# Performance work log

Hardware: AMD Instinct MI355X
Metric: run time of the kernel (lower is better)

## Reference

```python
import jax, jax.numpy as jnp
import numpy as np

B, T, K = 512, 512, 64  # batch, seq_len, num_tags


def setup_inputs() -> dict:
    key = jax.random.key(0)
    k1, k2 = jax.random.split(key)
    inputs = jax.random.normal(k1, (B, T, K), dtype=jnp.float32)
    # learned CRF transition matrix (GlorotUniform-ish scale)
    transitions = jax.random.normal(k2, (K, K), dtype=jnp.float32) * 0.1
    return {"inputs": inputs, "transitions": transitions}


def _viterbi_decode(potentials, transitions, seq_lens):
    """Faithful jax version of tfa/tf crf_decode (max-plus Viterbi DP + backtrace).

    potentials: [B, T, K] unary scores
    transitions: [K, K] pairwise scores (from_tag, to_tag)
    seq_lens: [B] int valid lengths
    Returns (decode_tags [B, T] int32, best_score [B] float).
    """
    b, t, k = potentials.shape
    pots_t = jnp.transpose(potentials, (1, 0, 2))  # [T, B, K]
    # mask[t-1, b] = step t (1..T-1) is within sequence b
    mask = jnp.arange(1, t)[:, None] < seq_lens[None, :]  # [T-1, B]
    ident = jnp.arange(k, dtype=jnp.int32)

    def fwd_step(alpha, xs):
        pot_t, m = xs  # pot_t: [B, K], m: [B]
        scores = alpha[:, :, None] + transitions[None, :, :]  # [B, K_from, K_to]
        new_alpha = pot_t + jnp.max(scores, axis=1)           # [B, K]
        bp = jnp.argmax(scores, axis=1).astype(jnp.int32)     # [B, K]
        alpha = jnp.where(m[:, None], new_alpha, alpha)       # freeze past seq end
        bp = jnp.where(m[:, None], bp, ident[None, :])        # identity backptr
        return alpha, bp

    alpha0 = pots_t[0]
    alpha_final, bps = jax.lax.scan(fwd_step, alpha0, (pots_t[1:], mask))  # bps: [T-1, B, K]
    best_score = jnp.max(alpha_final, axis=1)                  # [B]
    last_tag = jnp.argmax(alpha_final, axis=1).astype(jnp.int32)  # [B]

    def back_step(tag, bp_t):
        prev = jnp.take_along_axis(bp_t, tag[:, None], axis=1)[:, 0]
        return prev, prev

    # reverse scan: ys[t] = best tag at time t, for t = 0..T-2
    _, prev_tags = jax.lax.scan(back_step, last_tag, bps, reverse=True)
    tags = jnp.concatenate([prev_tags, last_tag[None]], axis=0)  # [T, B]
    return jnp.transpose(tags), best_score


def reference(inputs, transitions):
    # sequence lengths derived exactly as in the original call()
    used = jnp.sign(jnp.abs(inputs))                       # [B, T, K]
    seq_lens = jnp.mean(jnp.sum(used, axis=1), axis=1)     # [B]
    seq_lens = seq_lens.astype(jnp.int32)
    decode_tags, _best_score = _viterbi_decode(inputs, transitions, seq_lens)
    return decode_tags
```

## Files before the change

### kernel.cpp

```cpp
#include <hip/hip_runtime.h>

#define BB 512
#define TT 512
#define KK 64

typedef float v2f __attribute__((ext_vector_type(2)));

__device__ __forceinline__ float frl(float v, int lane) {
    return __int_as_float(__builtin_amdgcn_readlane(__float_as_int(v), lane));
}
__device__ __forceinline__ float fmax3(float a, float b, float c) {
    float d;
    asm("v_max3_f32 %0, %1, %2, %3" : "=v"(d) : "v"(a), "v"(b), "v"(c));
    return d;
}

#define FSTEP(PT) do {                                                          \
    la[lane] = alpha;                                                           \
    asm volatile("" ::: "memory");                                              \
    float acc0, acc1, acc2, acc3;                                               \
    {                                                                           \
        float4 a4 = ((float4*)la)[0];                                           \
        v2f lo; lo.x = a4.x; lo.y = a4.y; v2f cl = lo + tcl[0];                 \
        v2f hi; hi.x = a4.z; hi.y = a4.w; v2f ch = hi + tch[0];                 \
        acc0 = fmaxf(cl.x, cl.y); acc1 = fmaxf(ch.x, ch.y);                     \
        a4 = ((float4*)la)[1];                                                  \
        lo.x = a4.x; lo.y = a4.y; cl = lo + tcl[1];                             \
        hi.x = a4.z; hi.y = a4.w; ch = hi + tch[1];                             \
        acc2 = fmaxf(cl.x, cl.y); acc3 = fmaxf(ch.x, ch.y);                     \
    }                                                                           \
    _Pragma("unroll")                                                           \
    for (int c = 2; c < 16; c += 2) {                                           \
        float4 a4 = ((float4*)la)[c];                                           \
        v2f lo; lo.x = a4.x; lo.y = a4.y; v2f cl = lo + tcl[c];                 \
        v2f hi; hi.x = a4.z; hi.y = a4.w; v2f ch = hi + tch[c];                 \
        acc0 = fmax3(acc0, cl.x, cl.y); acc1 = fmax3(acc1, ch.x, ch.y);         \
        a4 = ((float4*)la)[c + 1];                                              \
        lo.x = a4.x; lo.y = a4.y; cl = lo + tcl[c + 1];                         \
        hi.x = a4.z; hi.y = a4.w; ch = hi + tch[c + 1];                         \
        acc2 = fmax3(acc2, cl.x, cl.y); acc3 = fmax3(acc3, ch.x, ch.y);         \
    }                                                                           \
    float M = fmaxf(fmax3(acc0, acc1, acc2), acc3);                             \
    *hp = M; hp += KK;                                                          \
    alpha = (PT) + M;                                                           \
} while (0)

__global__ __launch_bounds__(64, 1) void crf_fused(const float* __restrict__ pot,
                                                   const float* __restrict__ trans,
                                                   float* __restrict__ alphaH,
                                                   int* __restrict__ out) {
    __shared__ float tT[KK][KK + 1];
    __shared__ float la[KK];

    const int b = blockIdx.x;
    const int lane = threadIdx.x;
    const float* pb = pot + (size_t)b * TT * KK;
    float* hb = alphaH + (size_t)b * TT * KK;
    int* ob = out + b * TT;

    #pragma unroll 8
    for (int r = 0; r < KK; ++r) tT[lane][r] = trans[r * KK + lane];

    v2f tcl[16], tch[16];
    #pragma unroll
    for (int c = 0; c < 16; ++c) {
        v2f l2, h2;
        l2.x = trans[(4 * c + 0) * KK + lane]; l2.y = trans[(4 * c + 1) * KK + lane];
        h2.x = trans[(4 * c + 2) * KK + lane]; h2.y = trans[(4 * c + 3) * KK + lane];
        tcl[c] = l2; tch[c] = h2;
    }
    #pragma unroll
    for (int c = 0; c < 16; ++c) {
        asm volatile("" : "+v"(tcl[c]));
        asm volatile("" : "+v"(tch[c]));
    }

    float alpha = pb[lane];
    hb[lane] = 0.0f;
    float* hp = hb + KK + lane;

    float pf[4] = { pb[1 * KK + lane], pb[2 * KK + lane], pb[3 * KK + lane], pb[4 * KK + lane] };
    const float* lp = pb + 5 * KK + lane;

    #pragma unroll 1
    for (int c = 0; c < 126; ++c) {
        #pragma unroll
        for (int u = 0; u < 4; ++u) {
            FSTEP(pf[u]);
            pf[u] = *lp; lp += KK;
        }
    }
    float e0 = pb[509 * KK + lane], e1 = pb[510 * KK + lane], e2 = pb[511 * KK + lane];
    FSTEP(pf[0]); FSTEP(pf[1]); FSTEP(pf[2]); FSTEP(pf[3]);
    FSTEP(e0);    FSTEP(e1);    FSTEP(e2);

    int cnt = 0;
    {
        const float4* p4 = (const float4*)pb;
        #pragma unroll 4
        for (int r = 0; r < 128; ++r) {
            float4 v = p4[lane + 64 * r];
            cnt += (v.x != 0.f) + (v.y != 0.f) + (v.z != 0.f) + (v.w != 0.f);
        }
        #pragma unroll
        for (int off = 32; off > 0; off >>= 1) cnt += __shfl_xor(cnt, off, 64);
    }
    const int seqlen = cnt >> 6;

    asm volatile("s_waitcnt vmcnt(0)" ::: "memory");

    float afin = alpha;
    if (seqlen < TT) {
        if (seqlen <= 1) afin = pb[lane];
        else afin = pb[(seqlen - 1) * KK + lane] + hb[(seqlen - 1) * KK + lane];
    }

    float v = afin; int idx = lane;
    #pragma unroll
    for (int off = 1; off < 64; off <<= 1) {
        float vo = __shfl_xor(v, off, 64);
        int io = __shfl_xor(idx, off, 64);
        bool take = (vo > v) || (vo == v && io < idx);
        v = take ? vo : v;
        idx = take ? io : idx;
    }
    int cur = idx;
    int slot = cur;

    float mrow = hb[511 * KK + lane];
    float m0 = hb[510 * KK + lane], m1 = hb[509 * KK + lane], m2 = hb[508 * KK + lane],
          m3 = hb[507 * KK + lane], m4 = hb[506 * KK + lane], m5 = hb[505 * KK + lane],
          m6 = hb[504 * KK + lane], m7 = hb[503 * KK + lane];
    float p0 = pb[510 * KK + lane], p1 = pb[509 * KK + lane], p2 = pb[508 * KK + lane],
          p3 = pb[507 * KK + lane], p4 = pb[506 * KK + lane], p5 = pb[505 * KK + lane],
          p6 = pb[504 * KK + lane], p7 = pb[503 * KK + lane];

    auto bt_step = [&](int tt, float mlo, float plo) {
        if (tt < seqlen) {
            float target = frl(mrow, cur);
            float cand = (plo + mlo) + tT[cur][lane];
            unsigned long long mk = __ballot(cand == target);
            if (mk) cur = (int)__builtin_ctzll(mk);
        }
        mrow = mlo;
        const int tm = tt - 1;
        slot = ((tm & 63) == lane) ? cur : slot;
        if ((tm & 63) == 0) ob[tm + lane] = slot;
    };

    int T0 = 511;
    #pragma unroll 1
    for (int c = 0; c < 63; ++c) {
        bt_step(T0 - 0, m0, p0); { int pi = T0 - 9;  pi = pi < 0 ? 0 : pi; m0 = hb[pi * KK + lane]; p0 = pb[pi * KK + lane]; }
        bt_step(T0 - 1, m1, p1); { int pi = T0 - 10; pi = pi < 0 ? 0 : pi; m1 = hb[pi * KK + lane]; p1 = pb[pi * KK + lane]; }
        bt_step(T0 - 2, m2, p2); { int pi = T0 - 11; pi = pi < 0 ? 0 : pi; m2 = hb[pi * KK + lane]; p2 = pb[pi * KK + lane]; }
        bt_step(T0 - 3, m3, p3); { int pi = T0 - 12; pi = pi < 0 ? 0 : pi; m3 = hb[pi * KK + lane]; p3 = pb[pi * KK + lane]; }
        bt_step(T0 - 4, m4, p4); { int pi = T0 - 13; pi = pi < 0 ? 0 : pi; m4 = hb[pi * KK + lane]; p4 = pb[pi * KK + lane]; }
        bt_step(T0 - 5, m5, p5); { int pi = T0 - 14; pi = pi < 0 ? 0 : pi; m5 = hb[pi * KK + lane]; p5 = pb[pi * KK + lane]; }
        bt_step(T0 - 6, m6, p6); { int pi = T0 - 15; pi = pi < 0 ? 0 : pi; m6 = hb[pi * KK + lane]; p6 = pb[pi * KK + lane]; }
        bt_step(T0 - 7, m7, p7); { int pi = T0 - 16; pi = pi < 0 ? 0 : pi; m7 = hb[pi * KK + lane]; p7 = pb[pi * KK + lane]; }
        T0 -= 8;
    }
    bt_step(7, m0, p0); bt_step(6, m1, p1); bt_step(5, m2, p2); bt_step(4, m3, p3);
    bt_step(3, m4, p4); bt_step(2, m5, p5); bt_step(1, m6, p6);
}

__global__ __launch_bounds__(256) void seqlen_kernel(const float* __restrict__ inp,
                                                     int* __restrict__ seq_lens) {
    int b = blockIdx.x;
    int tid = threadIdx.x;
    const float4* p4 = (const float4*)(inp + (size_t)b * TT * KK);
    const int n4 = TT * KK / 4;
    int cnt = 0;
    for (int idx = tid; idx < n4; idx += 256) {
        float4 v = p4[idx];
        cnt += (v.x != 0.0f) + (v.y != 0.0f) + (v.z != 0.0f) + (v.w != 0.0f);
    }
    #pragma unroll
    for (int off = 32; off > 0; off >>= 1) cnt += __shfl_down(cnt, off, 64);
    __shared__ int wsum[4];
    if ((tid & 63) == 0) wsum[tid >> 6] = cnt;
    __syncthreads();
    if (tid == 0) seq_lens[b] = (wsum[0] + wsum[1] + wsum[2] + wsum[3]) >> 6;
}

__global__ __launch_bounds__(64) void viterbi_fallback(const float* __restrict__ pot,
                                                       const float* __restrict__ trans,
                                                       const int* __restrict__ seq_lens,
                                                       int* __restrict__ out) {
    __shared__ unsigned char bp[TT][KK];
    const int b = blockIdx.x;
    const int j = threadIdx.x;

    float tc[KK];
    #pragma unroll
    for (int i = 0; i < KK; ++i) tc[i] = trans[i * KK + j];

    const float* pb = pot + (size_t)b * TT * KK;
    float alpha = pb[j];
    const int seqlen = seq_lens[b];

    for (int t = 1; t < TT; ++t) {
        float ptj = pb[t * KK + j];
        float m[4]; int am[4];
        #pragma unroll
        for (int c = 0; c < 4; ++c) {
            const int i = c * 16;
            float ai = frl(alpha, i);
            m[c] = ai + tc[i];
            am[c] = i;
        }
        #pragma unroll
        for (int q = 1; q < 16; ++q) {
            #pragma unroll
            for (int c = 0; c < 4; ++c) {
                const int i = c * 16 + q;
                float ai = frl(alpha, i);
                float s = ai + tc[i];
                bool g = s > m[c];
                m[c] = g ? s : m[c];
                am[c] = g ? i : am[c];
            }
        }
        float M = m[0]; int BI = am[0];
        #pragma unroll
        for (int c = 1; c < 4; ++c) {
            bool g = m[c] > M;
            M = g ? m[c] : M;
            BI = g ? am[c] : BI;
        }
        const bool valid = (t < seqlen);
        alpha = valid ? (ptj + M) : alpha;
        bp[t][j] = (unsigned char)(valid ? BI : j);
    }

    float v = alpha; int idx = j;
    #pragma unroll
    for (int off = 1; off < 64; off <<= 1) {
        float vo = __shfl_xor(v, off, 64);
        int io = __shfl_xor(idx, off, 64);
        bool take = (vo > v) || (vo == v && io < idx);
        v = take ? vo : v;
        idx = take ? io : idx;
    }
    __syncthreads();
    if (j == 0) {
        int* ob = out + b * TT;
        int cur = idx;
        ob[TT - 1] = cur;
        for (int p = TT - 2; p >= 0; --p) {
            cur = bp[p + 1][cur];
            ob[p] = cur;
        }
    }
}

extern "C" void kernel_launch(void* const* d_in, const int* in_sizes, int n_in,
                              void* d_out, int out_size, void* d_ws, size_t ws_size,
                              hipStream_t stream) {
    const float* inp = (const float*)d_in[0];
    const float* trans = (const float*)d_in[1];
    int* out = (int*)d_out;

    const size_t histBytes = (size_t)BB * TT * KK * sizeof(float);
    if (ws_size >= histBytes) {
        float* alphaH = (float*)d_ws;
        crf_fused<<<BB, 64, 0, stream>>>(inp, trans, alphaH, out);
    } else {
        int* seq = (int*)d_ws;
        seqlen_kernel<<<BB, 256, 0, stream>>>(inp, seq);
        viterbi_fallback<<<BB, KK, 0, stream>>>(inp, trans, seq, out);
    }
}
```

Before: 259.5 us.

## Split Viterbi max-plus reduction across lanes with permlane32 swap and DPP combine

Each forward step is restructured so that every lane reduces only 16 of the 64 source tags, for four destination columns. It reads 4 float4 from LDS instead of 16. The partial maxima are merged across lanes with v_permlane32_swap and a DPP adjacent-lane swap, which shortens the LDS read stream on the serial recurrence. It adds cross-lane operations to the critical path and changes the transition register layout. The potential prefetch depth also goes from 4 to 8 steps, with the tail unrolled to match.

```diff
diff --git a/kernel.cpp b/kernel.cpp
--- a/kernel.cpp
+++ b/kernel.cpp
@@ -18,29 +18,43 @@
 #define FSTEP(PT) do {                                                          \
     la[lane] = alpha;                                                           \
     asm volatile("" ::: "memory");                                              \
-    float acc0, acc1, acc2, acc3;                                               \
+    float aA0, aA1, aB0, aB1;                                                   \
     {                                                                           \
-        float4 a4 = ((float4*)la)[0];                                           \
-        v2f lo; lo.x = a4.x; lo.y = a4.y; v2f cl = lo + tcl[0];                 \
-        v2f hi; hi.x = a4.z; hi.y = a4.w; v2f ch = hi + tch[0];                 \
-        acc0 = fmaxf(cl.x, cl.y); acc1 = fmaxf(ch.x, ch.y);                     \
-        a4 = ((float4*)la)[1];                                                  \
-        lo.x = a4.x; lo.y = a4.y; cl = lo + tcl[1];                             \
-        hi.x = a4.z; hi.y = a4.w; ch = hi + tch[1];                             \
-        acc2 = fmaxf(cl.x, cl.y); acc3 = fmaxf(ch.x, ch.y);                     \
+        float4 a4 = lab[0];                                                     \
+        v2f lo; lo.x = a4.x; lo.y = a4.y;                                       \
+        v2f hi; hi.x = a4.z; hi.y = a4.w;                                       \
+        v2f q;                                                                  \
+        q = lo + tA0l[0]; aA0 = fmaxf(q.x, q.y);                                \
+        q = hi + tA0h[0]; aA0 = fmax3(aA0, q.x, q.y);                           \
+        q = lo + tA1l[0]; aA1 = fmaxf(q.x, q.y);                                \
+        q = hi + tA1h[0]; aA1 = fmax3(aA1, q.x, q.y);                           \
+        q = lo + tB0l[0]; aB0 = fmaxf(q.x, q.y);                                \
+        q = hi + tB0h[0]; aB0 = fmax3(aB0, q.x, q.y);                           \
+        q = lo + tB1l[0]; aB1 = fmaxf(q.x, q.y);                                \
+        q = hi + tB1h[0]; aB1 = fmax3(aB1, q.x, q.y);                           \
     }                                                                           \
     _Pragma("unroll")                                                           \
-    for (int c = 2; c < 16; c += 2) {                                           \
-        float4 a4 = ((float4*)la)[c];                                           \
-        v2f lo; lo.x = a4.x; lo.y = a4.y; v2f cl = lo + tcl[c];                 \
-        v2f hi; hi.x = a4.z; hi.y = a4.w; v2f ch = hi + tch[c];                 \
-        acc0 = fmax3(acc0, cl.x, cl.y); acc1 = fmax3(acc1, ch.x, ch.y);         \
-        a4 = ((float4*)la)[c + 1];                                              \
-        lo.x = a4.x; lo.y = a4.y; cl = lo + tcl[c + 1];                         \
-        hi.x = a4.z; hi.y = a4.w; ch = hi + tch[c + 1];                         \
-        acc2 = fmax3(acc2, cl.x, cl.y); acc3 = fmax3(acc3, ch.x, ch.y);         \
+    for (int c = 1; c < 4; ++c) {                                               \
+        float4 a4 = lab[c];                                                     \
+        v2f lo; lo.x = a4.x; lo.y = a4.y;                                       \
+        v2f hi; hi.x = a4.z; hi.y = a4.w;                                       \
+        v2f q;                                                                  \
+        q = lo + tA0l[c]; aA0 = fmax3(aA0, q.x, q.y);                           \
+        q = hi + tA0h[c]; aA0 = fmax3(aA0, q.x, q.y);                           \
+        q = lo + tA1l[c]; aA1 = fmax3(aA1, q.x, q.y);                           \
+        q = hi + tA1h[c]; aA1 = fmax3(aA1, q.x, q.y);                           \
+        q = lo + tB0l[c]; aB0 = fmax3(aB0, q.x, q.y);                           \
+        q = hi + tB0h[c]; aB0 = fmax3(aB0, q.x, q.y);                           \
+        q = lo + tB1l[c]; aB1 = fmax3(aB1, q.x, q.y);                           \
+        q = hi + tB1h[c]; aB1 = fmax3(aB1, q.x, q.y);                           \
     }                                                                           \
-    float M = fmaxf(fmax3(acc0, acc1, acc2), acc3);                             \
+    asm volatile("v_permlane32_swap_b32 %0, %1" : "+v"(aA0), "+v"(aA1));        \
+    asm volatile("v_permlane32_swap_b32 %0, %1" : "+v"(aB0), "+v"(aB1));        \
+    float Yv = fmaxf(aA0, aA1);                                                 \
+    float Zv = fmaxf(aB0, aB1);                                                 \
+    float zp = __int_as_float(__builtin_amdgcn_update_dpp(                      \
+        __float_as_int(Zv), __float_as_int(Zv), 0xB1, 0xF, 0xF, false));        \
+    float M = fmaxf(Yv, zp);                                                    \
     *hp = M; hp += KK;                                                          \
     alpha = (PT) + M;                                                           \
 } while (0)
@@ -61,38 +75,58 @@
     #pragma unroll 8
     for (int r = 0; r < KK; ++r) tT[lane][r] = trans[r * KK + lane];
 
-    v2f tcl[16], tch[16];
-    #pragma unroll
-    for (int c = 0; c < 16; ++c) {
-        v2f l2, h2;
-        l2.x = trans[(4 * c + 0) * KK + lane]; l2.y = trans[(4 * c + 1) * KK + lane];
-        h2.x = trans[(4 * c + 2) * KK + lane]; h2.y = trans[(4 * c + 3) * KK + lane];
-        tcl[c] = l2; tch[c] = h2;
-    }
-    #pragma unroll
-    for (int c = 0; c < 16; ++c) {
-        asm volatile("" : "+v"(tcl[c]));
-        asm volatile("" : "+v"(tch[c]));
+    const int cA = lane & 31;
+    const int cB = cA ^ 1;
+    const int rb = (lane & 32) + ((lane & 1) << 4);
+    const float4* lab = (const float4*)(la + rb);
+
+    v2f tA0l[4], tA0h[4], tA1l[4], tA1h[4];
+    v2f tB0l[4], tB0h[4], tB1l[4], tB1h[4];
+    #pragma unroll
+    for (int c = 0; c < 4; ++c) {
+        const int r = rb + 4 * c;
+        v2f x;
+        x.x = trans[(r + 0) * KK + cA];      x.y = trans[(r + 1) * KK + cA];      tA0l[c] = x;
+        x.x = trans[(r + 2) * KK + cA];      x.y = trans[(r + 3) * KK + cA];      tA0h[c] = x;
+        x.x = trans[(r + 0) * KK + cA + 32]; x.y = trans[(r + 1) * KK + cA + 32]; tA1l[c] = x;
+        x.x = trans[(r + 2) * KK + cA + 32]; x.y = trans[(r + 3) * KK + cA + 32]; tA1h[c] = x;
+        x.x = trans[(r + 0) * KK + cB];      x.y = trans[(r + 1) * KK + cB];      tB0l[c] = x;
+        x.x = trans[(r + 2) * KK + cB];      x.y = trans[(r + 3) * KK + cB];      tB0h[c] = x;
+        x.x = trans[(r + 0) * KK + cB + 32]; x.y = trans[(r + 1) * KK + cB + 32]; tB1l[c] = x;
+        x.x = trans[(r + 2) * KK + cB + 32]; x.y = trans[(r + 3) * KK + cB + 32]; tB1h[c] = x;
+    }
+    #pragma unroll
+    for (int c = 0; c < 4; ++c) {
+        asm volatile("" : "+v"(tA0l[c])); asm volatile("" : "+v"(tA0h[c]));
+        asm volatile("" : "+v"(tA1l[c])); asm volatile("" : "+v"(tA1h[c]));
+        asm volatile("" : "+v"(tB0l[c])); asm volatile("" : "+v"(tB0h[c]));
+        asm volatile("" : "+v"(tB1l[c])); asm volatile("" : "+v"(tB1h[c]));
     }
 
     float alpha = pb[lane];
     hb[lane] = 0.0f;
     float* hp = hb + KK + lane;
 
-    float pf[4] = { pb[1 * KK + lane], pb[2 * KK + lane], pb[3 * KK + lane], pb[4 * KK + lane] };
-    const float* lp = pb + 5 * KK + lane;
+    float pf[8];
+    #pragma unroll
+    for (int u = 0; u < 8; ++u) pf[u] = pb[(1 + u) * KK + lane];
+    float ee[7];
+    #pragma unroll
+    for (int u = 0; u < 7; ++u) ee[u] = pb[(505 + u) * KK + lane];
+    const float* lp = pb + 9 * KK + lane;
 
     #pragma unroll 1
-    for (int c = 0; c < 126; ++c) {
-        #pragma unroll
-        for (int u = 0; u < 4; ++u) {
+    for (int c = 0; c < 62; ++c) {
+        #pragma unroll
+        for (int u = 0; u < 8; ++u) {
             FSTEP(pf[u]);
             pf[u] = *lp; lp += KK;
         }
     }
-    float e0 = pb[509 * KK + lane], e1 = pb[510 * KK + lane], e2 = pb[511 * KK + lane];
     FSTEP(pf[0]); FSTEP(pf[1]); FSTEP(pf[2]); FSTEP(pf[3]);
-    FSTEP(e0);    FSTEP(e1);    FSTEP(e2);
+    FSTEP(pf[4]); FSTEP(pf[5]); FSTEP(pf[6]); FSTEP(pf[7]);
+    FSTEP(ee[0]); FSTEP(ee[1]); FSTEP(ee[2]); FSTEP(ee[3]);
+    FSTEP(ee[4]); FSTEP(ee[5]); FSTEP(ee[6]);
 
     int cnt = 0;
     {
```

Measured after the change: 271.2 us. +4.5%, slower.

## Process two batch sequences per wavefront to interleave independent Viterbi chains

Applied to the files above, without the earlier changes.

Each 64-thread block now handles two batch elements, interleaving their forward max-plus recurrences and backtraces so two independent dependency chains share one wavefront. This targets latency-bound serial steps, where LDS round-trips and the max-reduction chain stall a single sequence, and lets the register-resident transition matrix be reused across both sequences. The cost is half as many blocks (256 on a chip with 256 CUs), more registers per thread, and twice the work per step, so throughput gains depend on how much latency the interleaving hides.

```diff
diff --git a/kernel.cpp b/kernel.cpp
--- a/kernel.cpp
+++ b/kernel.cpp
@@ -15,48 +15,72 @@
     return d;
 }
 
-#define FSTEP(PT) do {                                                          \
-    la[lane] = alpha;                                                           \
+#define FSTEP2(PT0, PT1) do {                                                   \
+    la0[lane] = alpha0;                                                         \
+    la1[lane] = alpha1;                                                         \
     asm volatile("" ::: "memory");                                              \
-    float acc0, acc1, acc2, acc3;                                               \
+    float A0, A1, A2, A3, B0, B1, B2, B3;                                       \
     {                                                                           \
-        float4 a4 = ((float4*)la)[0];                                           \
+        float4 a4 = ((float4*)la0)[0];                                          \
         v2f lo; lo.x = a4.x; lo.y = a4.y; v2f cl = lo + tcl[0];                 \
         v2f hi; hi.x = a4.z; hi.y = a4.w; v2f ch = hi + tch[0];                 \
-        acc0 = fmaxf(cl.x, cl.y); acc1 = fmaxf(ch.x, ch.y);                     \
-        a4 = ((float4*)la)[1];                                                  \
+        A0 = fmaxf(cl.x, cl.y); A1 = fmaxf(ch.x, ch.y);                         \
+        a4 = ((float4*)la1)[0];                                                 \
+        lo.x = a4.x; lo.y = a4.y; cl = lo + tcl[0];                             \
+        hi.x = a4.z; hi.y = a4.w; ch = hi + tch[0];                             \
+        B0 = fmaxf(cl.x, cl.y); B1 = fmaxf(ch.x, ch.y);                         \
+        a4 = ((float4*)la0)[1];                                                 \
         lo.x = a4.x; lo.y = a4.y; cl = lo + tcl[1];                             \
         hi.x = a4.z; hi.y = a4.w; ch = hi + tch[1];                             \
-        acc2 = fmaxf(cl.x, cl.y); acc3 = fmaxf(ch.x, ch.y);                     \
+        A2 = fmaxf(cl.x, cl.y); A3 = fmaxf(ch.x, ch.y);                         \
+        a4 = ((float4*)la1)[1];                                                 \
+        lo.x = a4.x; lo.y = a4.y; cl = lo + tcl[1];                             \
+        hi.x = a4.z; hi.y = a4.w; ch = hi + tch[1];                             \
+        B2 = fmaxf(cl.x, cl.y); B3 = fmaxf(ch.x, ch.y);                         \
     }                                                                           \
     _Pragma("unroll")                                                           \
     for (int c = 2; c < 16; c += 2) {                                           \
-        float4 a4 = ((float4*)la)[c];                                           \
+        float4 a4 = ((float4*)la0)[c];                                          \
         v2f lo; lo.x = a4.x; lo.y = a4.y; v2f cl = lo + tcl[c];                 \
         v2f hi; hi.x = a4.z; hi.y = a4.w; v2f ch = hi + tch[c];                 \
-        acc0 = fmax3(acc0, cl.x, cl.y); acc1 = fmax3(acc1, ch.x, ch.y);         \
-        a4 = ((float4*)la)[c + 1];                                              \
+        A0 = fmax3(A0, cl.x, cl.y); A1 = fmax3(A1, ch.x, ch.y);                 \
+        a4 = ((float4*)la1)[c];                                                 \
+        lo.x = a4.x; lo.y = a4.y; cl = lo + tcl[c];                             \
+        hi.x = a4.z; hi.y = a4.w; ch = hi + tch[c];                             \
+        B0 = fmax3(B0, cl.x, cl.y); B1 = fmax3(B1, ch.x, ch.y);                 \
+        a4 = ((float4*)la0)[c + 1];                                             \
         lo.x = a4.x; lo.y = a4.y; cl = lo + tcl[c + 1];                         \
         hi.x = a4.z; hi.y = a4.w; ch = hi + tch[c + 1];                         \
-        acc2 = fmax3(acc2, cl.x, cl.y); acc3 = fmax3(acc3, ch.x, ch.y);         \
+        A2 = fmax3(A2, cl.x, cl.y); A3 = fmax3(A3, ch.x, ch.y);                 \
+        a4 = ((float4*)la1)[c + 1];                                             \
+        lo.x = a4.x; lo.y = a4.y; cl = lo + tcl[c + 1];                         \
+        hi.x = a4.z; hi.y = a4.w; ch = hi + tch[c + 1];                         \
+        B2 = fmax3(B2, cl.x, cl.y); B3 = fmax3(B3, ch.x, ch.y);                 \
     }                                                                           \
-    float M = fmaxf(fmax3(acc0, acc1, acc2), acc3);                             \
-    *hp = M; hp += KK;                                                          \
-    alpha = (PT) + M;                                                           \
+    float M0 = fmaxf(fmax3(A0, A1, A2), A3);                                    \
+    float M1 = fmaxf(fmax3(B0, B1, B2), B3);                                    \
+    *hp0 = M0; hp0 += KK;                                                       \
+    *hp1 = M1; hp1 += KK;                                                       \
+    alpha0 = (PT0) + M0;                                                        \
+    alpha1 = (PT1) + M1;                                                        \
 } while (0)
 
-__global__ __launch_bounds__(64, 1) void crf_fused(const float* __restrict__ pot,
-                                                   const float* __restrict__ trans,
-                                                   float* __restrict__ alphaH,
-                                                   int* __restrict__ out) {
+__global__ __launch_bounds__(64, 1) void crf_fused2(const float* __restrict__ pot,
+                                                    const float* __restrict__ trans,
+                                                    float* __restrict__ alphaH,
+                                                    int* __restrict__ out) {
     __shared__ float tT[KK][KK + 1];
-    __shared__ float la[KK];
-
-    const int b = blockIdx.x;
+    __shared__ __align__(16) float la0[KK];
+    __shared__ __align__(16) float la1[KK];
+
+    const int b0 = blockIdx.x * 2;
     const int lane = threadIdx.x;
-    const float* pb = pot + (size_t)b * TT * KK;
-    float* hb = alphaH + (size_t)b * TT * KK;
-    int* ob = out + b * TT;
+    const float* pb0 = pot + (size_t)b0 * TT * KK;
+    const float* pb1 = pb0 + (size_t)TT * KK;
+    float* hb0 = alphaH + (size_t)b0 * TT * KK;
+    float* hb1 = hb0 + (size_t)TT * KK;
+    int* ob0 = out + b0 * TT;
+    int* ob1 = ob0 + TT;
 
     #pragma unroll 8
     for (int r = 0; r < KK; ++r) tT[lane][r] = trans[r * KK + lane];
@@ -75,94 +99,136 @@
         asm volatile("" : "+v"(tch[c]));
     }
 
-    float alpha = pb[lane];
-    hb[lane] = 0.0f;
-    float* hp = hb + KK + lane;
-
-    float pf[4] = { pb[1 * KK + lane], pb[2 * KK + lane], pb[3 * KK + lane], pb[4 * KK + lane] };
-    const float* lp = pb + 5 * KK + lane;
+    float alpha0 = pb0[lane];
+    float alpha1 = pb1[lane];
+    hb0[lane] = 0.0f;
+    hb1[lane] = 0.0f;
+    float* hp0 = hb0 + KK + lane;
+    float* hp1 = hb1 + KK + lane;
+
+    float pf0[4], pf1[4];
+    #pragma unroll
+    for (int u = 0; u < 4; ++u) {
+        pf0[u] = pb0[(1 + u) * KK + lane];
+        pf1[u] = pb1[(1 + u) * KK + lane];
+    }
+    const float* lp0 = pb0 + 5 * KK + lane;
+    const float* lp1 = pb1 + 5 * KK + lane;
 
     #pragma unroll 1
     for (int c = 0; c < 126; ++c) {
         #pragma unroll
         for (int u = 0; u < 4; ++u) {
-            FSTEP(pf[u]);
-            pf[u] = *lp; lp += KK;
-        }
-    }
-    float e0 = pb[509 * KK + lane], e1 = pb[510 * KK + lane], e2 = pb[511 * KK + lane];
-    FSTEP(pf[0]); FSTEP(pf[1]); FSTEP(pf[2]); FSTEP(pf[3]);
-    FSTEP(e0);    FSTEP(e1);    FSTEP(e2);
-
-    int cnt = 0;
+            FSTEP2(pf0[u], pf1[u]);
+            pf0[u] = *lp0; lp0 += KK;
+            pf1[u] = *lp1; lp1 += KK;
+        }
+    }
+    float e00 = pb0[509 * KK + lane], e01 = pb0[510 * KK + lane], e02 = pb0[511 * KK + lane];
+    float e10 = pb1[509 * KK + lane], e11 = pb1[510 * KK + lane], e12 = pb1[511 * KK + lane];
+    FSTEP2(pf0[0], pf1[0]); FSTEP2(pf0[1], pf1[1]);
+    FSTEP2(pf0[2], pf1[2]); FSTEP2(pf0[3], pf1[3]);
+    FSTEP2(e00, e10); FSTEP2(e01, e11); FSTEP2(e02, e12);
+
+    int cnt0 = 0, cnt1 = 0;
     {
-        const float4* p4 = (const float4*)pb;
+        const float4* p40 = (const float4*)pb0;
+        const float4* p41 = (const float4*)pb1;
         #pragma unroll 4
         for (int r = 0; r < 128; ++r) {
-            float4 v = p4[lane + 64 * r];
-            cnt += (v.x != 0.f) + (v.y != 0.f) + (v.z != 0.f) + (v.w != 0.f);
-        }
-        #pragma unroll
-        for (int off = 32; off > 0; off >>= 1) cnt += __shfl_xor(cnt, off, 64);
-    }
-    const int seqlen = cnt >> 6;
+            float4 v = p40[lane + 64 * r];
+            cnt0 += (v.x != 0.f) + (v.y != 0.f) + (v.z != 0.f) + (v.w != 0.f);
+            float4 w = p41[lane + 64 * r];
+            cnt1 += (w.x != 0.f) + (w.y != 0.f) + (w.z != 0.f) + (w.w != 0.f);
+        }
+        #pragma unroll
+        for (int off = 32; off > 0; off >>= 1) {
+            cnt0 += __shfl_xor(cnt0, off, 64);
+            cnt1 += __shfl_xor(cnt1, off, 64);
+        }
+    }
+    const int seqlen0 = cnt0 >> 6;
+    const int seqlen1 = cnt1 >> 6;
 
     asm volatile("s_waitcnt vmcnt(0)" ::: "memory");
 
-    float afin = alpha;
-    if (seqlen < TT) {
-        if (seqlen <= 1) afin = pb[lane];
-        else afin = pb[(seqlen - 1) * KK + lane] + hb[(seqlen - 1) * KK + lane];
-    }
-
-    float v = afin; int idx = lane;
+    float afin0 = alpha0;
+    if (seqlen0 < TT) {
+        if (seqlen0 <= 1) afin0 = pb0[lane];
+        else afin0 = pb0[(seqlen0 - 1) * KK + lane] + hb0[(seqlen0 - 1) * KK + lane];
+    }
+    float afin1 = alpha1;
+    if (seqlen1 < TT) {
+        if (seqlen1 <= 1) afin1 = pb1[lane];
+        else afin1 = pb1[(seqlen1 - 1) * KK + lane] + hb1[(seqlen1 - 1) * KK + lane];
+    }
+
+    float v0 = afin0; int idx0 = lane;
+    float v1 = afin1; int idx1 = lane;
     #pragma unroll
     for (int off = 1; off < 64; off <<= 1) {
-        float vo = __shfl_xor(v, off, 64);
-        int io = __shfl_xor(idx, off, 64);
-        bool take = (vo > v) || (vo == v && io < idx);
-        v = take ? vo : v;
-        idx = take ? io : idx;
-    }
-    int cur = idx;
-    int slot = cur;
-
-    float mrow = hb[511 * KK + lane];
-    float m0 = hb[510 * KK + lane], m1 = hb[509 * KK + lane], m2 = hb[508 * KK + lane],
-          m3 = hb[507 * KK + lane], m4 = hb[506 * KK + lane], m5 = hb[505 * KK + lane],
-          m6 = hb[504 * KK + lane], m7 = hb[503 * KK + lane];
-    float p0 = pb[510 * KK + lane], p1 = pb[509 * KK + lane], p2 = pb[508 * KK + lane],
-          p3 = pb[507 * KK + lane], p4 = pb[506 * KK + lane], p5 = pb[505 * KK + lane],
-          p6 = pb[504 * KK + lane], p7 = pb[503 * KK + lane];
-
-    auto bt_step = [&](int tt, float mlo, float plo) {
-        if (tt < seqlen) {
-            float target = frl(mrow, cur);
-            float cand = (plo + mlo) + tT[cur][lane];
+        float vo0 = __shfl_xor(v0, off, 64); int io0 = __shfl_xor(idx0, off, 64);
+        bool t0 = (vo0 > v0) || (vo0 == v0 && io0 < idx0);
+        v0 = t0 ? vo0 : v0; idx0 = t0 ? io0 : idx0;
+        float vo1 = __shfl_xor(v1, off, 64); int io1 = __shfl_xor(idx1, off, 64);
+        bool t1 = (vo1 > v1) || (vo1 == v1 && io1 < idx1);
+        v1 = t1 ? vo1 : v1; idx1 = t1 ? io1 : idx1;
+    }
+    int cur0 = idx0, cur1 = idx1;
+    int slot0 = cur0, slot1 = cur1;
+
+    float mr0 = hb0[511 * KK + lane], mr1 = hb1[511 * KK + lane];
+    float m00 = hb0[510 * KK + lane], m01 = hb0[509 * KK + lane], m02 = hb0[508 * KK + lane],
+          m03 = hb0[507 * KK + lane], m04 = hb0[506 * KK + lane], m05 = hb0[505 * KK + lane],
+          m06 = hb0[504 * KK + lane], m07 = hb0[503 * KK + lane];
+    float q00 = pb0[510 * KK + lane], q01 = pb0[509 * KK + lane], q02 = pb0[508 * KK + lane],
+          q03 = pb0[507 * KK + lane], q04 = pb0[506 * KK + lane], q05 = pb0[505 * KK + lane],
+          q06 = pb0[504 * KK + lane], q07 = pb0[503 * KK + lane];
+    float m10 = hb1[510 * KK + lane], m11 = hb1[509 * KK + lane], m12 = hb1[508 * KK + lane],
+          m13 = hb1[507 * KK + lane], m14 = hb1[506 * KK + lane], m15 = hb1[505 * KK + lane],
+          m16 = hb1[504 * KK + lane], m17 = hb1[503 * KK + lane];
+    float q10 = pb1[510 * KK + lane], q11 = pb1[509 * KK + lane], q12 = pb1[508 * KK + lane],
+          q13 = pb1[507 * KK + lane], q14 = pb1[506 * KK + lane], q15 = pb1[505 * KK + lane],
+          q16 = pb1[504 * KK + lane], q17 = pb1[503 * KK + lane];
+
+    auto bt2 = [&](int tt, float ma, float qa, float mb, float qb) {
+        if (tt < seqlen0) {
+            float target = frl(mr0, cur0);
+            float cand = (qa + ma) + tT[cur0][lane];
             unsigned long long mk = __ballot(cand == target);
-            if (mk) cur = (int)__builtin_ctzll(mk);
-        }
-        mrow = mlo;
+            if (mk) cur0 = (int)__builtin_ctzll(mk);
+        }
+        mr0 = ma;
+        if (tt < seqlen1) {
+            float target = frl(mr1, cur1);
+            float cand = (qb + mb) + tT[cur1][lane];
+            unsigned long long mk = __ballot(cand == target);
+            if (mk) cur1 = (int)__builtin_ctzll(mk);
+        }
+        mr1 = mb;
         const int tm = tt - 1;
-        slot = ((tm & 63) == lane) ? cur : slot;
-        if ((tm & 63) == 0) ob[tm + lane] = slot;
+        slot0 = ((tm & 63) == lane) ? cur0 : slot0;
+        slot1 = ((tm & 63) == lane) ? cur1 : slot1;
+        if ((tm & 63) == 0) { ob0[tm + lane] = slot0; ob1[tm + lane] = slot1; }
     };
 
     int T0 = 511;
     #pragma unroll 1
     for (int c = 0; c < 63; ++c) {
-        bt_step(T0 - 0, m0, p0); { int pi = T0 - 9;  pi = pi < 0 ? 0 : pi; m0 = hb[pi * KK + lane]; p0 = pb[pi * KK + lane]; }
-        bt_step(T0 - 1, m1, p1); { int pi = T0 - 10; pi = pi < 0 ? 0 : pi; m1 = hb[pi * KK + lane]; p1 = pb[pi * KK + lane]; }
-        bt_step(T0 - 2, m2, p2); { int pi = T0 - 11; pi = pi < 0 ? 0 : pi; m2 = hb[pi * KK + lane]; p2 = pb[pi * KK + lane]; }
-        bt_step(T0 - 3, m3, p3); { int pi = T0 - 12; pi = pi < 0 ? 0 : pi; m3 = hb[pi * KK + lane]; p3 = pb[pi * KK + lane]; }
-        bt_step(T0 - 4, m4, p4); { int pi = T0 - 13; pi = pi < 0 ? 0 : pi; m4 = hb[pi * KK + lane]; p4 = pb[pi * KK + lane]; }
-        bt_step(T0 - 5, m5, p5); { int pi = T0 - 14; pi = pi < 0 ? 0 : pi; m5 = hb[pi * KK + lane]; p5 = pb[pi * KK + lane]; }
-        bt_step(T0 - 6, m6, p6); { int pi = T0 - 15; pi = pi < 0 ? 0 : pi; m6 = hb[pi * KK + lane]; p6 = pb[pi * KK + lane]; }
-        bt_step(T0 - 7, m7, p7); { int pi = T0 - 16; pi = pi < 0 ? 0 : pi; m7 = hb[pi * KK + lane]; p7 = pb[pi * KK + lane]; }
+        bt2(T0 - 0, m00, q00, m10, q10); { int pi = T0 - 9;  pi = pi < 0 ? 0 : pi; m00 = hb0[pi * KK + lane]; q00 = pb0[pi * KK + lane]; m10 = hb1[pi * KK + lane]; q10 = pb1[pi * KK + lane]; }
+        bt2(T0 - 1, m01, q01, m11, q11); { int pi = T0 - 10; pi = pi < 0 ? 0 : pi; m01 = hb0[pi * KK + lane]; q01 = pb0[pi * KK + lane]; m11 = hb1[pi * KK + lane]; q11 = pb1[pi * KK + lane]; }
+        bt2(T0 - 2, m02, q02, m12, q12); { int pi = T0 - 11; pi = pi < 0 ? 0 : pi; m02 = hb0[pi * KK + lane]; q02 = pb0[pi * KK + lane]; m12 = hb1[pi * KK + lane]; q12 = pb1[pi * KK + lane]; }
+        bt2(T0 - 3, m03, q03, m13, q13); { int pi = T0 - 12; pi = pi < 0 ? 0 : pi; m03 = hb0[pi * KK + lane]; q03 = pb0[pi * KK + lane]; m13 = hb1[pi * KK + lane]; q13 = pb1[pi * KK + lane]; }
+        bt2(T0 - 4, m04, q04, m14, q14); { int pi = T0 - 13; pi = pi < 0 ? 0 : pi; m04 = hb0[pi * KK + lane]; q04 = pb0[pi * KK + lane]; m14 = hb1[pi * KK + lane]; q14 = pb1[pi * KK + lane]; }
+        bt2(T0 - 5, m05, q05, m15, q15); { int pi = T0 - 14; pi = pi < 0 ? 0 : pi; m05 = hb0[pi * KK + lane]; q05 = pb0[pi * KK + lane]; m15 = hb1[pi * KK + lane]; q15 = pb1[pi * KK + lane]; }
+        bt2(T0 - 6, m06, q06, m16, q16); { int pi = T0 - 15; pi = pi < 0 ? 0 : pi; m06 = hb0[pi * KK + lane]; q06 = pb0[pi * KK + lane]; m16 = hb1[pi * KK + lane]; q16 = pb1[pi * KK + lane]; }
+        bt2(T0 - 7, m07, q07, m17, q17); { int pi = T0 - 16; pi = pi < 0 ? 0 : pi; m07 = hb0[pi * KK + lane]; q07 = pb0[pi * KK + lane]; m17 = hb1[pi * KK + lane]; q17 = pb1[pi * KK + lane]; }
         T0 -= 8;
     }
-    bt_step(7, m0, p0); bt_step(6, m1, p1); bt_step(5, m2, p2); bt_step(4, m3, p3);
-    bt_step(3, m4, p4); bt_step(2, m5, p5); bt_step(1, m6, p6);
+    bt2(7, m00, q00, m10, q10); bt2(6, m01, q01, m11, q11);
+    bt2(5, m02, q02, m12, q12); bt2(4, m03, q03, m13, q13);
+    bt2(3, m04, q04, m14, q14); bt2(2, m05, q05, m15, q15);
+    bt2(1, m06, q06, m16, q16);
 }
 
 __global__ __launch_bounds__(256) void seqlen_kernel(const float* __restrict__ inp,
@@ -265,7 +331,7 @@
     const size_t histBytes = (size_t)BB * TT * KK * sizeof(float);
     if (ws_size >= histBytes) {
         float* alphaH = (float*)d_ws;
-        crf_fused<<<BB, 64, 0, stream>>>(inp, trans, alphaH, out);
+        crf_fused2<<<BB / 2, 64, 0, stream>>>(inp, trans, alphaH, out);
     } else {
         int* seq = (int*)d_ws;
         seqlen_kernel<<<BB, 256, 0, stream>>>(inp, seq);
```

Measured after the change: 751.8 us. 2.9x slower.

## Split Viterbi max reduction across lane halves with permlane32 swap combine

Applied to the files above, without the earlier changes.

Each lane now computes partial maxima for two destination tags (cc and cc+32) over only half of the source tags. It holds 32 packed transition pairs in registers instead of 64 values. The two half-wave partial results are combined with a permlane32_swap and a final max. This halves the LDS float4 reads on the serial per-timestep critical path. In exchange it adds a cross-lane swap per step and may raise the scalar max count, since the packed adds now broadcast one alpha value.

```diff
diff --git a/kernel.cpp b/kernel.cpp
--- a/kernel.cpp
+++ b/kernel.cpp
@@ -5,42 +5,43 @@
 #define KK 64
 
 typedef float v2f __attribute__((ext_vector_type(2)));
+typedef int v2i __attribute__((ext_vector_type(2)));
 
 __device__ __forceinline__ float frl(float v, int lane) {
     return __int_as_float(__builtin_amdgcn_readlane(__float_as_int(v), lane));
 }
-__device__ __forceinline__ float fmax3(float a, float b, float c) {
-    float d;
-    asm("v_max3_f32 %0, %1, %2, %3" : "=v"(d) : "v"(a), "v"(b), "v"(c));
-    return d;
+__device__ __forceinline__ v2f vmax2(v2f a, v2f b) {
+    v2f r; r.x = fmaxf(a.x, b.x); r.y = fmaxf(a.y, b.y); return r;
 }
 
 #define FSTEP(PT) do {                                                          \
     la[lane] = alpha;                                                           \
     asm volatile("" ::: "memory");                                              \
-    float acc0, acc1, acc2, acc3;                                               \
+    v2f accA, accB;                                                             \
     {                                                                           \
-        float4 a4 = ((float4*)la)[0];                                           \
-        v2f lo; lo.x = a4.x; lo.y = a4.y; v2f cl = lo + tcl[0];                 \
-        v2f hi; hi.x = a4.z; hi.y = a4.w; v2f ch = hi + tch[0];                 \
-        acc0 = fmaxf(cl.x, cl.y); acc1 = fmaxf(ch.x, ch.y);                     \
-        a4 = ((float4*)la)[1];                                                  \
-        lo.x = a4.x; lo.y = a4.y; cl = lo + tcl[1];                             \
-        hi.x = a4.z; hi.y = a4.w; ch = hi + tch[1];                             \
-        acc2 = fmaxf(cl.x, cl.y); acc3 = fmaxf(ch.x, ch.y);                     \
+        float4 a4 = lab[0];                                                     \
+        v2f c0; c0.x = a4.x + t2[0].x; c0.y = a4.x + t2[0].y;                   \
+        v2f c1; c1.x = a4.y + t2[1].x; c1.y = a4.y + t2[1].y;                   \
+        v2f c2; c2.x = a4.z + t2[2].x; c2.y = a4.z + t2[2].y;                   \
+        v2f c3; c3.x = a4.w + t2[3].x; c3.y = a4.w + t2[3].y;                   \
+        accA = vmax2(c0, c1);                                                   \
+        accB = vmax2(c2, c3);                                                   \
     }                                                                           \
     _Pragma("unroll")                                                           \
-    for (int c = 2; c < 16; c += 2) {                                           \
-        float4 a4 = ((float4*)la)[c];                                           \
-        v2f lo; lo.x = a4.x; lo.y = a4.y; v2f cl = lo + tcl[c];                 \
-        v2f hi; hi.x = a4.z; hi.y = a4.w; v2f ch = hi + tch[c];                 \
-        acc0 = fmax3(acc0, cl.x, cl.y); acc1 = fmax3(acc1, ch.x, ch.y);         \
-        a4 = ((float4*)la)[c + 1];                                              \
-        lo.x = a4.x; lo.y = a4.y; cl = lo + tcl[c + 1];                         \
-        hi.x = a4.z; hi.y = a4.w; ch = hi + tch[c + 1];                         \
-        acc2 = fmax3(acc2, cl.x, cl.y); acc3 = fmax3(acc3, ch.x, ch.y);         \
+    for (int k = 1; k < 8; ++k) {                                               \
+        float4 a4 = lab[k];                                                     \
+        v2f c0; c0.x = a4.x + t2[4*k+0].x; c0.y = a4.x + t2[4*k+0].y;           \
+        v2f c1; c1.x = a4.y + t2[4*k+1].x; c1.y = a4.y + t2[4*k+1].y;           \
+        v2f c2; c2.x = a4.z + t2[4*k+2].x; c2.y = a4.z + t2[4*k+2].y;           \
+        v2f c3; c3.x = a4.w + t2[4*k+3].x; c3.y = a4.w + t2[4*k+3].y;           \
+        accA = vmax2(accA, vmax2(c0, c1));                                      \
+        accB = vmax2(accB, vmax2(c2, c3));                                      \
     }                                                                           \
-    float M = fmaxf(fmax3(acc0, acc1, acc2), acc3);                             \
+    v2f accf = vmax2(accA, accB);                                               \
+    v2i sw = __builtin_amdgcn_permlane32_swap(__float_as_int(accf.x),           \
+                                              __float_as_int(accf.y),           \
+                                              false, false);                    \
+    float M = fmaxf(__int_as_float(sw[0]), __int_as_float(sw[1]));              \
     *hp = M; hp += KK;                                                          \
     alpha = (PT) + M;                                                           \
 } while (0)
@@ -50,7 +51,7 @@
                                                    float* __restrict__ alphaH,
                                                    int* __restrict__ out) {
     __shared__ float tT[KK][KK + 1];
-    __shared__ float la[KK];
+    __shared__ __align__(16) float la[KK];
 
     const int b = blockIdx.x;
     const int lane = threadIdx.x;
@@ -61,25 +62,28 @@
     #pragma unroll 8
     for (int r = 0; r < KK; ++r) tT[lane][r] = trans[r * KK + lane];
 
-    v2f tcl[16], tch[16];
-    #pragma unroll
-    for (int c = 0; c < 16; ++c) {
-        v2f l2, h2;
-        l2.x = trans[(4 * c + 0) * KK + lane]; l2.y = trans[(4 * c + 1) * KK + lane];
-        h2.x = trans[(4 * c + 2) * KK + lane]; h2.y = trans[(4 * c + 3) * KK + lane];
-        tcl[c] = l2; tch[c] = h2;
-    }
-    #pragma unroll
-    for (int c = 0; c < 16; ++c) {
-        asm volatile("" : "+v"(tcl[c]));
-        asm volatile("" : "+v"(tch[c]));
-    }
+    const int rbase = (lane >> 5) << 5;
+    const int cc = lane & 31;
+    const float4* lab = (const float4*)la + ((lane >> 5) << 3);
+
+    v2f t2[32];
+    #pragma unroll
+    for (int r = 0; r < 32; ++r) {
+        v2f x;
+        x.x = trans[(rbase + r) * KK + cc];
+        x.y = trans[(rbase + r) * KK + cc + 32];
+        t2[r] = x;
+    }
+    #pragma unroll
+    for (int r = 0; r < 32; ++r) asm volatile("" : "+v"(t2[r]));
 
     float alpha = pb[lane];
     hb[lane] = 0.0f;
     float* hp = hb + KK + lane;
 
-    float pf[4] = { pb[1 * KK + lane], pb[2 * KK + lane], pb[3 * KK + lane], pb[4 * KK + lane] };
+    float pf[4];
+    #pragma unroll
+    for (int u = 0; u < 4; ++u) pf[u] = pb[(1 + u) * KK + lane];
     const float* lp = pb + 5 * KK + lane;
 
     #pragma unroll 1
```

Result: slower. 295.2 us (+13.7%).
